# Kernel tuning notes

Hardware: AMD Instinct MI355X
Metric: run time of the kernel (lower is better)

The kernel has to match this reference:

```python
import jax, jax.numpy as jnp
import numpy as np

B, S, D, W, L = 16, 2048, 256, 8, 3


def _ln(x, g, b):
    # LayerNorm as in annotated-transformer SublayerConnection (eps=1e-6)
    m = jnp.mean(x, axis=-1, keepdims=True)
    v = jnp.var(x, axis=-1, keepdims=True)
    return g * (x - m) / jnp.sqrt(v + 1e-6) + b


def _ffn(x, w1, b1, w2, b2):
    # PositionwiseFeedForward: w2(relu(w1(x))), dropout off in eval
    return jax.nn.relu(x @ w1 + b1) @ w2 + b2


def setup_inputs() -> dict:
    key = jax.random.key(0)
    ks = jax.random.split(key, 16)
    s = 0.05
    inp = {
        "inputs": jax.random.normal(ks[0], (B, S, D), jnp.float32),
        "left_padding": jax.random.normal(ks[1], (W, D), jnp.float32) * s,
        "right_padding": jax.random.normal(ks[2], (W, D), jnp.float32) * s,
        "left_weights": jax.random.normal(ks[3], (W + 1,), jnp.float32) / (W + 1),
        "right_weights": jax.random.normal(ks[4], (W + 1,), jnp.float32) / (W + 1),
        "left_w1": jax.random.normal(ks[5], (L, D, D), jnp.float32) * s,
        "left_b1": jnp.zeros((L, D), jnp.float32),
        "left_w2": jax.random.normal(ks[6], (L, D, D), jnp.float32) * s,
        "left_b2": jnp.zeros((L, D), jnp.float32),
        "left_ln_g": jnp.ones((L, D), jnp.float32),
        "left_ln_b": jnp.zeros((L, D), jnp.float32),
        "right_w1": jax.random.normal(ks[7], (L, D, D), jnp.float32) * s,
        "right_b1": jnp.zeros((L, D), jnp.float32),
        "right_w2": jax.random.normal(ks[8], (L, D, D), jnp.float32) * s,
        "right_b2": jnp.zeros((L, D), jnp.float32),
        "right_ln_g": jnp.ones((L, D), jnp.float32),
        "right_ln_b": jnp.zeros((L, D), jnp.float32),
    }
    return inp


def reference(inputs, left_padding, right_padding, left_weights, right_weights,
              left_w1, left_b1, left_w2, left_b2, left_ln_g, left_ln_b,
              right_w1, right_b1, right_w2, right_b2, right_ln_g, right_ln_b):
    b, s, d = inputs.shape
    w = left_padding.shape[0]
    nl = left_w1.shape[0]
    # pad with learned boundary vectors: (b, w + s + w, d)
    padded = jnp.concatenate([
        jnp.broadcast_to(left_padding, (b, w, d)),
        inputs,
        jnp.broadcast_to(right_padding, (b, w, d)),
    ], axis=1)
    # vectorized unfold replacing the per-position python loop:
    idx = jnp.arange(s)[:, None] + jnp.arange(w + 1)[None, :]  # (s, w+1)
    left_win = padded[:, idx]        # (b, s, w+1, d): tokens t-w .. t
    right_win = padded[:, idx + w]   # (b, s, w+1, d): tokens t .. t+w
    left_out = jnp.einsum('bswd,w->bsd', left_win, left_weights)
    right_out = jnp.einsum('bswd,w->bsd', right_win, right_weights)
    layers = []
    for i in range(nl):
        # SublayerConnection: x + FFN(LN(x))
        left_out = left_out + _ffn(_ln(left_out, left_ln_g[i], left_ln_b[i]),
                                   left_w1[i], left_b1[i], left_w2[i], left_b2[i])
        right_out = right_out + _ffn(_ln(right_out, right_ln_g[i], right_ln_b[i]),
                                     right_w1[i], right_b1[i], right_w2[i], right_b2[i])
        layers.append(jnp.concatenate([left_out, right_out], axis=-1))  # (b, s, 2d)
    all_layers = jnp.stack(layers, axis=0)  # (nl, b, s, 2d)
    return all_layers, layers[-1]
```

## Files before the change

### kernel.cpp

```cpp
#include <hip/hip_runtime.h>

typedef __attribute__((ext_vector_type(8))) short bf16x8;
typedef __attribute__((ext_vector_type(4))) float f32x4;

#define UR _Pragma("unroll")

__device__ __forceinline__ float bf2f(unsigned short u) {
    union { unsigned int i; float f; } v; v.i = ((unsigned int)u) << 16; return v.f;
}
__device__ __forceinline__ unsigned short f2bf(float f) {
    union { float f; unsigned int i; } v; v.f = f;
    unsigned int u = v.i;
    return (unsigned short)((u + 0x7FFFu + ((u >> 16) & 1u)) >> 16);
}
__device__ __forceinline__ uint2 pack4(f32x4 x) {
    uint2 o;
    o.x = (unsigned int)f2bf(x[0]) | ((unsigned int)f2bf(x[1]) << 16);
    o.y = (unsigned int)f2bf(x[2]) | ((unsigned int)f2bf(x[3]) << 16);
    return o;
}
__device__ __forceinline__ int swz(int r, int c) {
    return r * 512 + (c ^ ((r & 7) << 4));
}

__global__ __launch_bounds__(256)
void prep_kernel(const float* __restrict__ lw1, const float* __restrict__ rw1,
                 const float* __restrict__ lw2, const float* __restrict__ rw2,
                 unsigned short* __restrict__ w1t, unsigned short* __restrict__ w2t)
{
    __shared__ unsigned short T[64][68];
    int bid = blockIdx.x;
    int mat = bid >> 4;
    int tile = bid & 15;
    int tensor = mat / 3;
    int l = mat - tensor * 3;
    int k0 = (tile >> 2) * 64, n0 = (tile & 3) * 64;
    const float* src = (tensor == 0) ? lw1 : (tensor == 1) ? rw1 : (tensor == 2) ? lw2 : rw2;
    unsigned short* dst = ((tensor < 2) ? w1t : w2t) + (tensor & 1) * 196608;

    int tx = threadIdx.x & 63, ty = threadIdx.x >> 6;
    UR for (int p = 0; p < 16; ++p) {
        int k = k0 + p * 4 + ty;
        T[tx][k - k0] = f2bf(src[l * 65536 + k * 256 + n0 + tx]);
    }
    __syncthreads();
    UR for (int p = 0; p < 16; ++p) {
        int n = n0 + p * 4 + ty;
        dst[l * 65536 + n * 256 + k0 + tx] = T[n - n0][tx];
    }
}

__global__ __launch_bounds__(256, 4)
void conv_kernel(const float* __restrict__ inp,
                 const float* __restrict__ lpad, const float* __restrict__ rpad,
                 const float* __restrict__ lwt, const float* __restrict__ rwt,
                 uint2* __restrict__ wsL, uint2* __restrict__ wsR)
{
    int raw = blockIdx.x;
    int w = (raw & 7) * 128 + (raw >> 3);
    int t = threadIdx.x;
    int q = t & 63;
    int g = t >> 6;
    int R0 = w * 32 + g * 8;
    int s0 = R0 & 2047;
    int c = q * 4;

    float wl[9], wr[9];
    UR for (int j = 0; j < 9; ++j) { wl[j] = lwt[j]; wr[j] = rwt[j]; }

    f32x4 aL[8], aR[8];
    UR for (int k = 0; k < 8; ++k) {
        aL[k] = (f32x4){0.f, 0.f, 0.f, 0.f};
        aR[k] = (f32x4){0.f, 0.f, 0.f, 0.f};
    }
    UR for (int i = -8; i <= 15; ++i) {
        int si = s0 + i;
        const float* src;
        if (si < 0)          src = lpad + (si + 8) * 256 + c;
        else if (si >= 2048) src = rpad + (si - 2048) * 256 + c;
        else                 src = inp + (size_t)(R0 + i) * 256 + c;
        f32x4 v = *(const f32x4*)src;
        UR for (int k = 0; k < 8; ++k) {
            int j = i - k;
            if (j >= -8 && j <= 0) aL[k] += v * wl[j + 8];
            if (j >= 0 && j <= 8)  aR[k] += v * wr[j];
        }
    }
    UR for (int k = 0; k < 8; ++k) {
        int idx = (R0 + k) * 64 + q;
        wsL[idx] = pack4(aL[k]);
        wsR[idx] = pack4(aR[k]);
    }
}

__global__ __launch_bounds__(256, 4)
void mega_kernel(const unsigned short* __restrict__ convbf,
                 const unsigned short* __restrict__ w1t,
                 const unsigned short* __restrict__ w2t,
                 const float* __restrict__ b1L, const float* __restrict__ b1R,
                 const float* __restrict__ b2L, const float* __restrict__ b2R,
                 const float* __restrict__ gL,  const float* __restrict__ gR,
                 const float* __restrict__ bbL, const float* __restrict__ bbR,
                 float* __restrict__ out)
{
    __shared__ unsigned short YH[32 * 256];
    __shared__ float red[4][32][2];

    const int t = threadIdx.x;
    const int wm = t >> 6;
    const int ln = t & 63;
    const int lr = ln & 15;
    const int lh = ln >> 4;

    const int raw = blockIdx.x;
    const int w = (raw & 7) * 256 + (raw >> 3);
    const int br = w >> 10;
    const int tile = w & 1023;
    const int r0 = tile * 32;

    const unsigned short* cv  = convbf + (size_t)br * (32768u * 256u);
    const unsigned short* W1b = w1t + (size_t)br * 196608;
    const unsigned short* W2b = w2t + (size_t)br * 196608;
    const float* B1 = br ? b1R : b1L;
    const float* B2 = br ? b2R : b2L;
    const float* G  = br ? gR  : gL;
    const float* Bb = br ? bbR : bbL;

    int rr[2], dd[4], hh[4];
    UR for (int n = 0; n < 2; ++n) rr[n] = n * 16 + lr;
    UR for (int m = 0; m < 4; ++m) dd[m] = wm * 64 + m * 16 + lh * 4;
    UR for (int m = 0; m < 4; ++m) hh[m] = wm * 64 + m * 16 + lr;

    f32x4 x[4][2];
    UR for (int m = 0; m < 4; ++m)
      UR for (int n = 0; n < 2; ++n) {
        uint2 raw2 = *(const uint2*)(cv + (size_t)(r0 + rr[n]) * 256 + dd[m]);
        f32x4 v;
        v[0] = bf2f((unsigned short)(raw2.x & 0xffffu));
        v[1] = bf2f((unsigned short)(raw2.x >> 16));
        v[2] = bf2f((unsigned short)(raw2.y & 0xffffu));
        v[3] = bf2f((unsigned short)(raw2.y >> 16));
        x[m][n] = v;
      }

    for (int lay = 0; lay < 3; ++lay) {
        UR for (int n = 0; n < 2; ++n) {
            float s = 0.f, q = 0.f;
            UR for (int m = 0; m < 4; ++m)
              UR for (int r = 0; r < 4; ++r) { float v = x[m][n][r]; s += v; q += v * v; }
            s += __shfl_xor(s, 16); q += __shfl_xor(q, 16);
            s += __shfl_xor(s, 32); q += __shfl_xor(q, 32);
            if (lh == 0) {
                red[wm][n * 16 + lr][0] = s;
                red[wm][n * 16 + lr][1] = q;
            }
        }
        __syncthreads();
        float mean[2], rstd[2];
        UR for (int n = 0; n < 2; ++n) {
            int row = n * 16 + lr;
            float S = 0.f, Q = 0.f;
            UR for (int u = 0; u < 4; ++u) { S += red[u][row][0]; Q += red[u][row][1]; }
            float mu = S * (1.f / 256.f);
            float var = Q * (1.f / 256.f) - mu * mu;
            mean[n] = mu;
            rstd[n] = rsqrtf(var + 1e-6f);
        }
        f32x4 gf[4], bfr_[4];
        UR for (int m = 0; m < 4; ++m) {
            gf[m]   = *(const f32x4*)(G  + lay * 256 + dd[m]);
            bfr_[m] = *(const f32x4*)(Bb + lay * 256 + dd[m]);
        }
        UR for (int m = 0; m < 4; ++m)
          UR for (int n = 0; n < 2; ++n) {
            f32x4 y;
            UR for (int r = 0; r < 4; ++r)
                y[r] = (x[m][n][r] - mean[n]) * rstd[n] * gf[m][r] + bfr_[m][r];
            *(uint2*)((char*)YH + swz(rr[n], dd[m] * 2)) = pack4(y);
          }
        __syncthreads();

        const unsigned short* Wl = W1b + lay * 65536;
        f32x4 acc[4][2];
        UR for (int m = 0; m < 4; ++m)
          UR for (int n = 0; n < 2; ++n) acc[m][n] = (f32x4){0.f, 0.f, 0.f, 0.f};
        UR for (int kk = 0; kk < 8; ++kk) {
            bf16x8 a[4], b[2];
            UR for (int m = 0; m < 4; ++m)
                a[m] = *(const bf16x8*)(Wl + hh[m] * 256 + kk * 32 + lh * 8);
            UR for (int n = 0; n < 2; ++n)
                b[n] = *(const bf16x8*)((const char*)YH + swz(rr[n], kk * 64 + lh * 16));
            UR for (int m = 0; m < 4; ++m)
              UR for (int n = 0; n < 2; ++n)
                acc[m][n] = __builtin_amdgcn_mfma_f32_16x16x32_bf16(a[m], b[n], acc[m][n], 0, 0, 0);
        }
        f32x4 b1f[4];
        UR for (int m = 0; m < 4; ++m) b1f[m] = *(const f32x4*)(B1 + lay * 256 + dd[m]);
        __syncthreads();
        UR for (int m = 0; m < 4; ++m)
          UR for (int n = 0; n < 2; ++n) {
            f32x4 h;
            UR for (int r = 0; r < 4; ++r) h[r] = fmaxf(acc[m][n][r] + b1f[m][r], 0.f);
            *(uint2*)((char*)YH + swz(rr[n], dd[m] * 2)) = pack4(h);
          }
        __syncthreads();

        const unsigned short* W2l = W2b + lay * 65536;
        UR for (int m = 0; m < 4; ++m)
          UR for (int n = 0; n < 2; ++n) acc[m][n] = (f32x4){0.f, 0.f, 0.f, 0.f};
        UR for (int kk = 0; kk < 8; ++kk) {
            bf16x8 a[4], b[2];
            UR for (int m = 0; m < 4; ++m)
                a[m] = *(const bf16x8*)(W2l + hh[m] * 256 + kk * 32 + lh * 8);
            UR for (int n = 0; n < 2; ++n)
                b[n] = *(const bf16x8*)((const char*)YH + swz(rr[n], kk * 64 + lh * 16));
            UR for (int m = 0; m < 4; ++m)
              UR for (int n = 0; n < 2; ++n)
                acc[m][n] = __builtin_amdgcn_mfma_f32_16x16x32_bf16(a[m], b[n], acc[m][n], 0, 0, 0);
        }
        f32x4 b2f[4];
        UR for (int m = 0; m < 4; ++m) b2f[m] = *(const f32x4*)(B2 + lay * 256 + dd[m]);
        UR for (int m = 0; m < 4; ++m)
          UR for (int n = 0; n < 2; ++n)
            UR for (int r = 0; r < 4; ++r)
                x[m][n][r] += acc[m][n][r] + b2f[m][r];

        float* outL = out + ((size_t)lay * 32768 + r0) * 512 + br * 256;
        UR for (int m = 0; m < 4; ++m)
          UR for (int n = 0; n < 2; ++n) {
            float* p = outL + (size_t)rr[n] * 512 + dd[m];
            *(f32x4*)p = x[m][n];
            if (lay == 2) *(f32x4*)(p + 16777216) = x[m][n];
          }
    }
}

extern "C" void kernel_launch(void* const* d_in, const int* in_sizes, int n_in,
                              void* d_out, int out_size, void* d_ws, size_t ws_size,
                              hipStream_t stream)
{
    const float* inputs = (const float*)d_in[0];
    const float* lpad = (const float*)d_in[1];
    const float* rpad = (const float*)d_in[2];
    const float* lwt  = (const float*)d_in[3];
    const float* rwt  = (const float*)d_in[4];
    const float* lw1  = (const float*)d_in[5];
    const float* lb1  = (const float*)d_in[6];
    const float* lw2  = (const float*)d_in[7];
    const float* lb2  = (const float*)d_in[8];
    const float* lg   = (const float*)d_in[9];
    const float* lbb  = (const float*)d_in[10];
    const float* rw1  = (const float*)d_in[11];
    const float* rb1  = (const float*)d_in[12];
    const float* rw2  = (const float*)d_in[13];
    const float* rb2  = (const float*)d_in[14];
    const float* rg   = (const float*)d_in[15];
    const float* rbb  = (const float*)d_in[16];

    char* ws = (char*)d_ws;
    unsigned short* convb = (unsigned short*)ws;
    unsigned short* w1t   = (unsigned short*)(ws + 33554432);
    unsigned short* w2t   = (unsigned short*)(ws + 33554432 + 786432);

    prep_kernel<<<192, 256, 0, stream>>>(lw1, rw1, lw2, rw2, w1t, w2t);
    conv_kernel<<<1024, 256, 0, stream>>>(inputs, lpad, rpad, lwt, rwt,
                                          (uint2*)convb, (uint2*)(convb + 32768u * 256u));
    mega_kernel<<<2048, 256, 0, stream>>>(convb, w1t, w2t,
                                          lb1, rb1, lb2, rb2, lg, rg, lbb, rbb,
                                          (float*)d_out);
}
```

Measured before the change: 550.7 us.

## Stream pre-swizzled weight slices into LDS with double-buffered async loads

The prep kernel now writes the FFN weights as bf16 slices already laid out in MFMA fragment order. The main kernel doubles its tile to 64 rows with 512 threads, so each weight slice is reused by two waves. Weights are staged into a double-buffered LDS ring with global_load_lds, and the load for the next slice is issued while the current one is consumed. This replaces per-wave strided global weight loads with shared, prefetched loads, at the cost of more LDS, more barriers and hand-written waitcnt accounting that must match the number of outstanding loads.

Result: faster. 441.4 us (-19.8%).

```diff
diff --git a/kernel.cpp b/kernel.cpp
--- a/kernel.cpp
+++ b/kernel.cpp
@@ -4,6 +4,11 @@
 typedef __attribute__((ext_vector_type(4))) float f32x4;
 
 #define UR _Pragma("unroll")
+#define LGKM0 asm volatile("s_waitcnt lgkmcnt(0)" ::: "memory")
+#define BARRIER do { LGKM0; __builtin_amdgcn_s_barrier(); } while (0)
+#define WAITV2  asm volatile("s_waitcnt vmcnt(2)" ::: "memory")
+#define WAITV10 asm volatile("s_waitcnt vmcnt(10)" ::: "memory")
+#define WAITV0  asm volatile("s_waitcnt vmcnt(0)" ::: "memory")
 
 __device__ __forceinline__ float bf2f(unsigned short u) {
     union { unsigned int i; float f; } v; v.i = ((unsigned int)u) << 16; return v.f;
@@ -26,27 +31,32 @@
 __global__ __launch_bounds__(256)
 void prep_kernel(const float* __restrict__ lw1, const float* __restrict__ rw1,
                  const float* __restrict__ lw2, const float* __restrict__ rw2,
-                 unsigned short* __restrict__ w1t, unsigned short* __restrict__ w2t)
+                 unsigned short* __restrict__ wstream)
 {
-    __shared__ unsigned short T[64][68];
+    __shared__ float T[8192];
     int bid = blockIdx.x;
-    int mat = bid >> 4;
-    int tile = bid & 15;
-    int tensor = mat / 3;
-    int l = mat - tensor * 3;
-    int k0 = (tile >> 2) * 64, n0 = (tile & 3) * 64;
-    const float* src = (tensor == 0) ? lw1 : (tensor == 1) ? rw1 : (tensor == 2) ? lw2 : rw2;
-    unsigned short* dst = ((tensor < 2) ? w1t : w2t) + (tensor & 1) * 196608;
-
-    int tx = threadIdx.x & 63, ty = threadIdx.x >> 6;
-    UR for (int p = 0; p < 16; ++p) {
-        int k = k0 + p * 4 + ty;
-        T[tx][k - k0] = f2bf(src[l * 65536 + k * 256 + n0 + tx]);
-    }
+    int s = bid & 7, G = (bid >> 3) & 1, lay = (bid >> 4) % 3, br = bid / 48;
+    const float* src = (G == 0) ? (br ? rw1 : lw1) : (br ? rw2 : lw2);
+    src += lay * 65536 + s * 8192;
+    int t = threadIdx.x;
+    UR for (int i = 0; i < 32; ++i) T[i * 256 + t] = src[i * 256 + t];
     __syncthreads();
-    UR for (int p = 0; p < 16; ++p) {
-        int n = n0 + p * 4 + ty;
-        dst[l * 65536 + n * 256 + k0 + tx] = T[n - n0][tx];
+    int S = lay * 16 + G * 8 + s;
+    unsigned short* dst = wstream + (size_t)br * 393216 + S * 8192 + t * 32;
+    UR for (int c = 0; c < 4; ++c) {
+        unsigned int wv[4];
+        UR for (int h = 0; h < 4; ++h) {
+            unsigned short e2[2];
+            UR for (int z = 0; z < 2; ++z) {
+                int f = t * 32 + c * 8 + h * 2 + z;
+                int grp = f >> 9, lh = (f >> 7) & 3, lr = (f >> 3) & 15, e = f & 7;
+                int n = grp * 16 + lr, kl = lh * 8 + e;
+                e2[z] = f2bf(T[kl * 256 + n]);
+            }
+            wv[h] = (unsigned int)e2[0] | ((unsigned int)e2[1] << 16);
+        }
+        uint4 v; v.x = wv[0]; v.y = wv[1]; v.z = wv[2]; v.w = wv[3];
+        *(uint4*)(dst + c * 8) = v;
     }
 }
 
@@ -93,57 +103,72 @@
     }
 }
 
-__global__ __launch_bounds__(256, 4)
+__device__ __forceinline__ void stage_slice(const unsigned short* g, unsigned short* l, int t) {
+    __builtin_amdgcn_global_load_lds(
+        (const __attribute__((address_space(1))) unsigned int*)(g + t * 8),
+        (__attribute__((address_space(3))) unsigned int*)(l + t * 8), 16, 0, 0);
+    __builtin_amdgcn_global_load_lds(
+        (const __attribute__((address_space(1))) unsigned int*)(g + 4096 + t * 8),
+        (__attribute__((address_space(3))) unsigned int*)(l + 4096 + t * 8), 16, 0, 0);
+}
+
+__global__ __launch_bounds__(512, 4)
 void mega_kernel(const unsigned short* __restrict__ convbf,
-                 const unsigned short* __restrict__ w1t,
-                 const unsigned short* __restrict__ w2t,
+                 const unsigned short* __restrict__ wstream,
                  const float* __restrict__ b1L, const float* __restrict__ b1R,
                  const float* __restrict__ b2L, const float* __restrict__ b2R,
                  const float* __restrict__ gL,  const float* __restrict__ gR,
                  const float* __restrict__ bbL, const float* __restrict__ bbR,
                  float* __restrict__ out)
 {
-    __shared__ unsigned short YH[32 * 256];
-    __shared__ float red[4][32][2];
+    __shared__ unsigned short Ybuf[64 * 256];
+    __shared__ unsigned short WSH[2 * 8192];
+    __shared__ float red[4][64][2];
 
     const int t = threadIdx.x;
-    const int wm = t >> 6;
+    const int wv2 = t >> 6;
     const int ln = t & 63;
     const int lr = ln & 15;
     const int lh = ln >> 4;
+    const int wm = wv2 >> 1;
+    const int wn = wv2 & 1;
 
     const int raw = blockIdx.x;
-    const int w = (raw & 7) * 256 + (raw >> 3);
-    const int br = w >> 10;
-    const int tile = w & 1023;
-    const int r0 = tile * 32;
+    const int w = (raw & 7) * 128 + (raw >> 3);
+    const int br = w >> 9;
+    const int r0 = (w & 511) * 64;
 
     const unsigned short* cv  = convbf + (size_t)br * (32768u * 256u);
-    const unsigned short* W1b = w1t + (size_t)br * 196608;
-    const unsigned short* W2b = w2t + (size_t)br * 196608;
+    const unsigned short* Wst = wstream + (size_t)br * 393216;
     const float* B1 = br ? b1R : b1L;
     const float* B2 = br ? b2R : b2L;
     const float* G  = br ? gR  : gL;
     const float* Bb = br ? bbR : bbL;
 
-    int rr[2], dd[4], hh[4];
-    UR for (int n = 0; n < 2; ++n) rr[n] = n * 16 + lr;
+    int rr[2], dd[4], aoff[4];
+    UR for (int n = 0; n < 2; ++n) rr[n] = wn * 32 + n * 16 + lr;
     UR for (int m = 0; m < 4; ++m) dd[m] = wm * 64 + m * 16 + lh * 4;
-    UR for (int m = 0; m < 4; ++m) hh[m] = wm * 64 + m * 16 + lr;
+    UR for (int m = 0; m < 4; ++m) aoff[m] = ((wm * 4 + m) * 64 + ln) * 8;
 
     f32x4 x[4][2];
     UR for (int m = 0; m < 4; ++m)
       UR for (int n = 0; n < 2; ++n) {
-        uint2 raw2 = *(const uint2*)(cv + (size_t)(r0 + rr[n]) * 256 + dd[m]);
+        uint2 rw2_ = *(const uint2*)(cv + (size_t)(r0 + rr[n]) * 256 + dd[m]);
         f32x4 v;
-        v[0] = bf2f((unsigned short)(raw2.x & 0xffffu));
-        v[1] = bf2f((unsigned short)(raw2.x >> 16));
-        v[2] = bf2f((unsigned short)(raw2.y & 0xffffu));
-        v[3] = bf2f((unsigned short)(raw2.y >> 16));
+        v[0] = bf2f((unsigned short)(rw2_.x & 0xffffu));
+        v[1] = bf2f((unsigned short)(rw2_.x >> 16));
+        v[2] = bf2f((unsigned short)(rw2_.y & 0xffffu));
+        v[3] = bf2f((unsigned short)(rw2_.y >> 16));
         x[m][n] = v;
       }
+    stage_slice(Wst, WSH, t);
 
     for (int lay = 0; lay < 3; ++lay) {
+        f32x4 gf[4], bfr_[4];
+        UR for (int m = 0; m < 4; ++m) {
+            gf[m]   = *(const f32x4*)(G  + lay * 256 + dd[m]);
+            bfr_[m] = *(const f32x4*)(Bb + lay * 256 + dd[m]);
+        }
         UR for (int n = 0; n < 2; ++n) {
             float s = 0.f, q = 0.f;
             UR for (int m = 0; m < 4; ++m)
@@ -151,73 +176,80 @@
             s += __shfl_xor(s, 16); q += __shfl_xor(q, 16);
             s += __shfl_xor(s, 32); q += __shfl_xor(q, 32);
             if (lh == 0) {
-                red[wm][n * 16 + lr][0] = s;
-                red[wm][n * 16 + lr][1] = q;
+                red[wm][rr[n]][0] = s;
+                red[wm][rr[n]][1] = q;
             }
         }
-        __syncthreads();
-        float mean[2], rstd[2];
-        UR for (int n = 0; n < 2; ++n) {
-            int row = n * 16 + lr;
-            float S = 0.f, Q = 0.f;
-            UR for (int u = 0; u < 4; ++u) { S += red[u][row][0]; Q += red[u][row][1]; }
-            float mu = S * (1.f / 256.f);
-            float var = Q * (1.f / 256.f) - mu * mu;
-            mean[n] = mu;
-            rstd[n] = rsqrtf(var + 1e-6f);
-        }
-        f32x4 gf[4], bfr_[4];
-        UR for (int m = 0; m < 4; ++m) {
-            gf[m]   = *(const f32x4*)(G  + lay * 256 + dd[m]);
-            bfr_[m] = *(const f32x4*)(Bb + lay * 256 + dd[m]);
-        }
-        UR for (int m = 0; m < 4; ++m)
-          UR for (int n = 0; n < 2; ++n) {
-            f32x4 y;
-            UR for (int r = 0; r < 4; ++r)
-                y[r] = (x[m][n][r] - mean[n]) * rstd[n] * gf[m][r] + bfr_[m][r];
-            *(uint2*)((char*)YH + swz(rr[n], dd[m] * 2)) = pack4(y);
-          }
-        __syncthreads();
-
-        const unsigned short* Wl = W1b + lay * 65536;
+
         f32x4 acc[4][2];
         UR for (int m = 0; m < 4; ++m)
           UR for (int n = 0; n < 2; ++n) acc[m][n] = (f32x4){0.f, 0.f, 0.f, 0.f};
+
         UR for (int kk = 0; kk < 8; ++kk) {
+            int S = lay * 16 + kk;
+            BARRIER;
+            stage_slice(Wst + (S + 1) * 8192, WSH + ((S + 1) & 1) * 8192, t);
+            if (kk == 0) {
+                float mean[2], rstd[2];
+                UR for (int n = 0; n < 2; ++n) {
+                    float Ssum = 0.f, Q = 0.f;
+                    UR for (int u = 0; u < 4; ++u) { Ssum += red[u][rr[n]][0]; Q += red[u][rr[n]][1]; }
+                    float mu = Ssum * (1.f / 256.f);
+                    mean[n] = mu;
+                    rstd[n] = rsqrtf(Q * (1.f / 256.f) - mu * mu + 1e-6f);
+                }
+                UR for (int m = 0; m < 4; ++m)
+                  UR for (int n = 0; n < 2; ++n) {
+                    f32x4 y;
+                    UR for (int r = 0; r < 4; ++r)
+                        y[r] = (x[m][n][r] - mean[n]) * rstd[n] * gf[m][r] + bfr_[m][r];
+                    *(uint2*)((char*)Ybuf + swz(rr[n], dd[m] * 2)) = pack4(y);
+                  }
+            }
+            if (lay > 0 && kk == 0) { WAITV10; } else { WAITV2; }
+            BARRIER;
+            const unsigned short* bufp = WSH + (S & 1) * 8192;
             bf16x8 a[4], b[2];
-            UR for (int m = 0; m < 4; ++m)
-                a[m] = *(const bf16x8*)(Wl + hh[m] * 256 + kk * 32 + lh * 8);
+            UR for (int m = 0; m < 4; ++m) a[m] = *(const bf16x8*)(bufp + aoff[m]);
             UR for (int n = 0; n < 2; ++n)
-                b[n] = *(const bf16x8*)((const char*)YH + swz(rr[n], kk * 64 + lh * 16));
+                b[n] = *(const bf16x8*)((const char*)Ybuf + swz(rr[n], kk * 64 + lh * 16));
             UR for (int m = 0; m < 4; ++m)
               UR for (int n = 0; n < 2; ++n)
                 acc[m][n] = __builtin_amdgcn_mfma_f32_16x16x32_bf16(a[m], b[n], acc[m][n], 0, 0, 0);
         }
+
         f32x4 b1f[4];
         UR for (int m = 0; m < 4; ++m) b1f[m] = *(const f32x4*)(B1 + lay * 256 + dd[m]);
-        __syncthreads();
+        uint2 hp[4][2];
         UR for (int m = 0; m < 4; ++m)
           UR for (int n = 0; n < 2; ++n) {
             f32x4 h;
             UR for (int r = 0; r < 4; ++r) h[r] = fmaxf(acc[m][n][r] + b1f[m][r], 0.f);
-            *(uint2*)((char*)YH + swz(rr[n], dd[m] * 2)) = pack4(h);
+            hp[m][n] = pack4(h);
+            acc[m][n] = (f32x4){0.f, 0.f, 0.f, 0.f};
           }
-        __syncthreads();
-
-        const unsigned short* W2l = W2b + lay * 65536;
-        UR for (int m = 0; m < 4; ++m)
-          UR for (int n = 0; n < 2; ++n) acc[m][n] = (f32x4){0.f, 0.f, 0.f, 0.f};
+
         UR for (int kk = 0; kk < 8; ++kk) {
+            int S = lay * 16 + 8 + kk;
+            BARRIER;
+            if (S < 47) stage_slice(Wst + (S + 1) * 8192, WSH + ((S + 1) & 1) * 8192, t);
+            if (kk == 0) {
+                UR for (int m = 0; m < 4; ++m)
+                  UR for (int n = 0; n < 2; ++n)
+                    *(uint2*)((char*)Ybuf + swz(rr[n], dd[m] * 2)) = hp[m][n];
+            }
+            if (S == 47) { WAITV0; } else { WAITV2; }
+            BARRIER;
+            const unsigned short* bufp = WSH + (S & 1) * 8192;
             bf16x8 a[4], b[2];
-            UR for (int m = 0; m < 4; ++m)
-                a[m] = *(const bf16x8*)(W2l + hh[m] * 256 + kk * 32 + lh * 8);
+            UR for (int m = 0; m < 4; ++m) a[m] = *(const bf16x8*)(bufp + aoff[m]);
             UR for (int n = 0; n < 2; ++n)
-                b[n] = *(const bf16x8*)((const char*)YH + swz(rr[n], kk * 64 + lh * 16));
+                b[n] = *(const bf16x8*)((const char*)Ybuf + swz(rr[n], kk * 64 + lh * 16));
             UR for (int m = 0; m < 4; ++m)
               UR for (int n = 0; n < 2; ++n)
                 acc[m][n] = __builtin_amdgcn_mfma_f32_16x16x32_bf16(a[m], b[n], acc[m][n], 0, 0, 0);
         }
+
         f32x4 b2f[4];
         UR for (int m = 0; m < 4; ++m) b2f[m] = *(const f32x4*)(B2 + lay * 256 + dd[m]);
         UR for (int m = 0; m < 4; ++m)
@@ -259,13 +291,12 @@
 
     char* ws = (char*)d_ws;
     unsigned short* convb = (unsigned short*)ws;
-    unsigned short* w1t   = (unsigned short*)(ws + 33554432);
-    unsigned short* w2t   = (unsigned short*)(ws + 33554432 + 786432);
-
-    prep_kernel<<<192, 256, 0, stream>>>(lw1, rw1, lw2, rw2, w1t, w2t);
+    unsigned short* wstr  = (unsigned short*)(ws + 33554432);
+
+    prep_kernel<<<96, 256, 0, stream>>>(lw1, rw1, lw2, rw2, wstr);
     conv_kernel<<<1024, 256, 0, stream>>>(inputs, lpad, rpad, lwt, rwt,
                                           (uint2*)convb, (uint2*)(convb + 32768u * 256u));
-    mega_kernel<<<2048, 256, 0, stream>>>(convb, w1t, w2t,
+    mega_kernel<<<1024, 512, 0, stream>>>(convb, wstr,
                                           lb1, rb1, lb2, rb2, lg, rg, lbb, rbb,
                                           (float*)d_out);
 }
```
